# Performance work log

Measured on AMD Instinct MI355X. Metric: run time of the kernel, lower is better.

## Reference

```python
import jax, jax.numpy as jnp
import numpy as np

N = 100_000          # nodes
E = 3_200_000        # edges (avg degree 32)
NEG_SLOPE = 0.2      # PyG GATConv default


def _gat_conv(x, src, dst, W, a_src, a_dst, b, n):
    """Single-head PyG-style GATConv. src/dst already include self-loops."""
    h = x @ W                                   # [N, F_out]
    logits = (h @ a_src)[src] + (h @ a_dst)[dst]  # [E']
    e = jax.nn.leaky_relu(logits, NEG_SLOPE)
    m = jax.ops.segment_max(e, dst, num_segments=n)
    ex = jnp.exp(e - m[dst])                    # stable ragged softmax over in-edges
    s = jax.ops.segment_sum(ex, dst, num_segments=n)
    alpha = ex / (s[dst] + 1e-16)
    out = jax.ops.segment_sum(h[src] * alpha[:, None], dst, num_segments=n)
    return out + b


def setup_inputs() -> dict:
    key = jax.random.key(0)
    ks = jax.random.split(key, 20)
    x = jax.random.normal(ks[0], (N, 3), dtype=jnp.float32)
    edge_index = jax.random.randint(ks[1], (2, E), 0, N, dtype=jnp.int64)

    def lin(k, fin, fout):
        return jax.random.normal(k, (fin, fout), dtype=jnp.float32) * (1.0 / np.sqrt(fin))

    def att(k, f):
        return jax.random.normal(k, (f,), dtype=jnp.float32) * (1.0 / np.sqrt(f))

    inp = {"x": x, "edge_index": edge_index}
    # forward-direction convs
    inp["W1"], inp["as1"], inp["ad1"], inp["b1"] = lin(ks[2], 3, 16), att(ks[3], 16), att(ks[4], 16), jnp.zeros((16,), jnp.float32)
    inp["W2"], inp["as2"], inp["ad2"], inp["b2"] = lin(ks[5], 16, 1), att(ks[6], 1), att(ks[7], 1), jnp.zeros((1,), jnp.float32)
    # reverse-direction convs
    inp["W1r"], inp["as1r"], inp["ad1r"], inp["b1r"] = lin(ks[8], 3, 16), att(ks[9], 16), att(ks[10], 16), jnp.zeros((16,), jnp.float32)
    inp["W2r"], inp["as2r"], inp["ad2r"], inp["b2r"] = lin(ks[11], 16, 1), att(ks[12], 1), att(ks[13], 1), jnp.zeros((1,), jnp.float32)
    return inp


def reference(x, edge_index, W1, as1, ad1, b1, W2, as2, ad2, b2,
              W1r, as1r, ad1r, b1r, W2r, as2r, ad2r, b2r):
    n = x.shape[0]
    loops = jnp.arange(n, dtype=edge_index.dtype)
    # forward direction (self-loops appended, as PyG add_self_loops=True)
    src = jnp.concatenate([edge_index[0], loops])
    dst = jnp.concatenate([edge_index[1], loops])
    # reverse direction: stack([ei[1], ei[0]]) then self-loops
    rsrc = jnp.concatenate([edge_index[1], loops])
    rdst = jnp.concatenate([edge_index[0], loops])

    xf = jax.nn.relu(_gat_conv(x, src, dst, W1, as1, ad1, b1, n))
    xf = _gat_conv(xf, src, dst, W2, as2, ad2, b2, n)

    xr = jax.nn.relu(_gat_conv(x, rsrc, rdst, W1r, as1r, ad1r, b1r, n))
    xr = _gat_conv(xr, rsrc, rdst, W2r, as2r, ad2r, b2r, n)

    return (xf + xr) * 0.5
```

## Files before the change

kernel.cpp:

```cpp
#include <hip/hip_runtime.h>
#include <math.h>

#define NSLOPE 0.2f
#define BSH 8
#define BNODES 256
#define NID_MASK 0x1FFFF
#define SENT 0xFFFFFFFFu
#define CAP 9216
#define GB2 768
#define RT 512
#define EPT2 9
#define REDG (RT * EPT2)
#define RREC (2 * REDG)
#define BN8 256
#define BAG2T 512
#define CPP2 9

__device__ __forceinline__ float lrelu(float v) { return v > 0.f ? v : NSLOPE * v; }

__global__ void k_prep(const float* __restrict__ x,
                       const float* __restrict__ as1, const float* __restrict__ ad1,
                       const float* __restrict__ as1r, const float* __restrict__ ad1r,
                       const float* __restrict__ W1, const float* __restrict__ W1r,
                       float4* __restrict__ rec4f, float4* __restrict__ rec4r,
                       float* __restrict__ s1df, float* __restrict__ s1dr,
                       int* __restrict__ gcur, int NS, int N) {
    int i = blockIdx.x * blockDim.x + threadIdx.x;
    if (i < NS) gcur[i] = 0;
    if (i >= N) return;
    float x0 = x[3 * i], x1 = x[3 * i + 1], x2 = x[3 * i + 2];
    float ssf = 0.f, sdf = 0.f, ssr = 0.f, sdr = 0.f;
#pragma unroll
    for (int k = 0; k < 16; k++) {
        float hf = x0 * W1[k] + x1 * W1[16 + k] + x2 * W1[32 + k];
        ssf += hf * as1[k];
        sdf += hf * ad1[k];
        float hr = x0 * W1r[k] + x1 * W1r[16 + k] + x2 * W1r[32 + k];
        ssr += hr * as1r[k];
        sdr += hr * ad1r[k];
    }
    rec4f[i] = make_float4(x0, x1, x2, ssf);
    rec4r[i] = make_float4(x0, x1, x2, ssr);
    s1df[i] = sdf; s1dr[i] = sdr;
}

__global__ void __launch_bounds__(RT, 6) k_scatsort(
        const void* __restrict__ ei, long long E,
        int NB, int NS, int* __restrict__ gcur, unsigned* __restrict__ bin) {
    extern __shared__ unsigned smem[];
    unsigned* rec = smem;
    int* cnt  = (int*)(rec + RREC);
    int* loff = cnt + NS;
    int* gbs  = loff + NS;
    int* wtot = gbs + NS;
    __shared__ int flagsm;

    int t = threadIdx.x;
    if (t < 64) {
        const unsigned long long* p = (const unsigned long long*)ei;
        bool bad = false;
#pragma unroll
        for (int i = 0; i < 4; i++)
            if (p[t * 4 + i] >= (1ull << 32)) bad = true;
        unsigned long long mask = __ballot(bad);
        if (t == 0) flagsm = (mask == 0ull) ? 1 : 0;
    }
    __syncthreads();
    int fl = flagsm;
    long long chunk = (E + GB2 - 1) / GB2;
    long long cstart = (long long)blockIdx.x * chunk;
    long long cend = cstart + chunk; if (cend > E) cend = E;
    int rot = (int)((blockIdx.x * 197u) % (unsigned)NS);

    for (long long rs = cstart; rs < cend; rs += REDG) {
        int ne = (int)min((long long)REDG, cend - rs);
        for (int i = t; i < NS; i += RT) cnt[i] = 0;
        int eu[EPT2], ev[EPT2];
#pragma unroll
        for (int k = 0; k < EPT2; k++) {
            int idx = t + k * RT;
            eu[k] = -1;
            if (idx < ne) {
                long long i = rs + idx;
                if (fl) { const long long* p = (const long long*)ei;
                          eu[k] = (int)p[i]; ev[k] = (int)p[E + i]; }
                else    { const int* p = (const int*)ei;
                          eu[k] = p[i]; ev[k] = p[E + i]; }
            }
        }
        __syncthreads();
#pragma unroll
        for (int k = 0; k < EPT2; k++) {
            if (eu[k] >= 0) {
                atomicAdd(&cnt[ev[k] >> BSH], 1);
                atomicAdd(&cnt[NB + (eu[k] >> BSH)], 1);
            }
        }
        __syncthreads();
        int base = 0;
        for (int st = 0; st < NS; st += RT) {
            int idx = st + t;
            int val = (idx < NS) ? cnt[idx] : 0;
            int lane = t & 63, wv = t >> 6;
            int incl = val;
#pragma unroll
            for (int od = 1; od < 64; od <<= 1) {
                int up = __shfl_up(incl, od);
                if (lane >= od) incl += up;
            }
            if (lane == 63) wtot[wv] = incl;
            __syncthreads();
            int woff = 0;
#pragma unroll
            for (int j = 0; j < 8; j++) woff += (j < wv) ? wtot[j] : 0;
            if (idx < NS) {
                int lo = base + woff + incl - val;
                loff[idx] = lo;
                cnt[idx] = lo;
                gbs[idx] = val ? atomicAdd(&gcur[idx], val) : 0;
            }
            int stot = 0;
#pragma unroll
            for (int j = 0; j < 8; j++) stot += wtot[j];
            base += stot;
            __syncthreads();
        }
#pragma unroll
        for (int k = 0; k < EPT2; k++) {
            if (eu[k] >= 0) {
                int u = eu[k], v = ev[k];
                unsigned r0 = (unsigned)u | ((unsigned)(v & (BNODES - 1)) << 17);
                int s0 = v >> BSH;
                int p0 = atomicAdd(&cnt[s0], 1);
                rec[p0] = r0;
                unsigned r1 = (unsigned)v | ((unsigned)(u & (BNODES - 1)) << 17);
                int s1 = NB + (u >> BSH);
                int p1 = atomicAdd(&cnt[s1], 1);
                rec[p1] = r1;
            }
        }
        __syncthreads();
        for (int i = t; i < NS; i += RT) {
            int s = i + rot; if (s >= NS) s -= NS;
            int ls = loff[s], le = cnt[s];
            int n = le - ls;
            if (!n) continue;
            int g = gbs[s];
            if (g >= CAP) continue;
            if (g + n > CAP) n = CAP - g;
            long long b = (long long)s * CAP;
            int j = 0;
            if (g & 1) { bin[b + g] = rec[ls]; j = 1; }
            if (((g + j) & 2) && j + 2 <= n) {
                *(uint2*)(bin + b + g + j) = make_uint2(rec[ls + j], rec[ls + j + 1]);
                j += 2;
            }
            for (; j + 4 <= n; j += 4)
                *(uint4*)(bin + b + g + j) =
                    make_uint4(rec[ls + j], rec[ls + j + 1],
                               rec[ls + j + 2], rec[ls + j + 3]);
            if (j + 2 <= n) {
                *(uint2*)(bin + b + g + j) = make_uint2(rec[ls + j], rec[ls + j + 1]);
                j += 2;
            }
            if (j < n) bin[b + g + j] = rec[ls + j];
        }
        __syncthreads();
    }
}

__global__ void __launch_bounds__(BAG2T, 8) k_bagg1(
        unsigned* __restrict__ bin, const int* __restrict__ gcur,
        const float4* __restrict__ rec4f, const float* __restrict__ s1df,
        const float4* __restrict__ rec4r, const float* __restrict__ s1dr,
        const float* __restrict__ b1, const float* __restrict__ W1,
        const float* __restrict__ W2,
        const float* __restrict__ as2, const float* __restrict__ ad2,
        const float* __restrict__ b1r, const float* __restrict__ W1r,
        const float* __restrict__ W2r,
        const float* __restrict__ as2r, const float* __restrict__ ad2r,
        float2* __restrict__ p2f, float* __restrict__ s2df,
        float2* __restrict__ p2r, float* __restrict__ s2dr,
        int* __restrict__ aoff, int* __restrict__ aend, int NB8, int N) {
    int bb = blockIdx.x, dir = blockIdx.y;
    const float4* rec4 = dir ? rec4r : rec4f;
    const float* s1d = dir ? s1dr : s1df;
    const float* b1_ = dir ? b1r : b1;
    const float* W1_ = dir ? W1r : W1;
    const float* W2_ = dir ? W2r : W2;
    float as2v = dir ? as2r[0] : as2[0];
    float ad2v = dir ? ad2r[0] : ad2[0];
    float2* p2 = dir ? p2r : p2f;
    float* s2d = dir ? s2dr : s2df;

    int c0 = dir * NB8 + bb;
    long long base = (long long)c0 * CAP;
    int n0 = gcur[c0]; if (n0 > CAP) n0 = CAP;
    int np0 = (n0 + 1) >> 1;
    int v0 = bb << BSH;
    int nv = N - v0; if (nv > BN8) nv = BN8;

    __shared__ int cnt[BN8];
    __shared__ int loff[BN8];
    __shared__ int segtot[4];
    __shared__ unsigned lds_u[CAP];
    int t = threadIdx.x;

    const uint2* bp0 = (const uint2*)(bin + base);
    uint2 recs[CPP2];
#pragma unroll
    for (int k = 0; k < CPP2; k++) {
        int i = t + k * BAG2T;
        uint2 r = make_uint2(SENT, SENT);
        if (i < np0) {
            r = bp0[i];
            if (2 * i + 1 >= n0) r.y = SENT;
        }
        recs[k] = r;
    }
    if (t < BN8) cnt[t] = 0;
    __syncthreads();
#pragma unroll
    for (int k = 0; k < CPP2; k++) {
        if (recs[k].x != SENT) atomicAdd(&cnt[recs[k].x >> 17], 1);
        if (recs[k].y != SENT) atomicAdd(&cnt[recs[k].y >> 17], 1);
    }
    __syncthreads();
    if (t < BN8) {
        int lane = t & 63, wv = t >> 6;
        int val = cnt[t];
        int incl = val;
#pragma unroll
        for (int od = 1; od < 64; od <<= 1) {
            int up = __shfl_up(incl, od);
            if (lane >= od) incl += up;
        }
        if (lane == 63) segtot[wv] = incl;
        loff[t] = incl - val;
    }
    __syncthreads();
    if (t < BN8) {
        int wv = t >> 6;
        int offs = 0;
#pragma unroll
        for (int j = 0; j < 4; j++) offs += (j < wv) ? segtot[j] : 0;
        int ex = loff[t] + offs;
        loff[t] = ex;
        cnt[t] = ex;
    }
    __syncthreads();
#pragma unroll
    for (int k = 0; k < CPP2; k++) {
        if (recs[k].x != SENT) {
            int q = atomicAdd(&cnt[recs[k].x >> 17], 1);
            lds_u[q] = recs[k].x & NID_MASK;
        }
        if (recs[k].y != SENT) {
            int q = atomicAdd(&cnt[recs[k].y >> 17], 1);
            lds_u[q] = recs[k].y & NID_MASK;
        }
    }
    __syncthreads();
    int node = t >> 1, lane = t & 1;
    float sdv = (node < nv) ? s1d[v0 + node] : 0.f;
    float d = 0.f, a0 = 0.f, a1 = 0.f, a2 = 0.f;
    if (node < nv) {
        int ls = loff[node], le = cnt[node];
        for (int pos = ls + lane; pos < le; pos += 2) {
            unsigned u = lds_u[pos];
            float4 r = rec4[u];
            float w = __expf(lrelu(r.w + sdv));
            d += w; a0 += w * r.x; a1 += w * r.y; a2 += w * r.z;
        }
    }
    d  += __shfl_xor(d, 1);
    a0 += __shfl_xor(a0, 1);
    a1 += __shfl_xor(a1, 1);
    a2 += __shfl_xor(a2, 1);
    if (lane == 0 && node < nv) {
        int v = v0 + node;
        float4 r = rec4[v];
        float w = __expf(lrelu(r.w + sdv));
        float dd = d + w;
        float inv = 1.f / (dd + 1e-16f);
        float m0 = (a0 + w * r.x) * inv;
        float m1 = (a1 + w * r.y) * inv;
        float m2 = (a2 + w * r.z) * inv;
        float h2v = 0.f;
#pragma unroll
        for (int k = 0; k < 16; k++) {
            float o = m0 * W1_[k] + m1 * W1_[16 + k] + m2 * W1_[32 + k] + b1_[k];
            o = fmaxf(o, 0.f);
            h2v += o * W2_[k];
        }
        p2[v] = make_float2(h2v, h2v * as2v);
        s2d[v] = h2v * ad2v;
    }
    int nreal = cnt[BN8 - 1];
    if (t == 0 && (nreal & 1)) lds_u[nreal] = SENT;
    __syncthreads();
    int ndp = (nreal + 1) >> 1;
    uint2* bq = (uint2*)(bin + base);
    for (int i = t; i < ndp; i += BAG2T)
        bq[i] = make_uint2(lds_u[2 * i], lds_u[2 * i + 1]);
    if (t < nv) {
        aoff[dir * N + v0 + t] = (int)(base + loff[t]);
        aend[dir * N + v0 + t] = (int)(base + cnt[t]);
    }
}

__global__ void k_agg2(const unsigned* __restrict__ bin,
                       const int* __restrict__ aoff, const int* __restrict__ aend,
                       const float2* __restrict__ p2f, const float* __restrict__ s2df,
                       const float2* __restrict__ p2r, const float* __restrict__ s2dr,
                       const float* __restrict__ b2, const float* __restrict__ b2r,
                       float* __restrict__ out, int N) {
    int tid = blockIdx.x * blockDim.x + threadIdx.x;
    int v = tid >> 4;
    int lane = tid & 15;
    if (v >= N) return;
    float res[2];
#pragma unroll
    for (int dir = 0; dir < 2; dir++) {
        const float2* p2 = dir ? p2r : p2f;
        const float* s2d = dir ? s2dr : s2df;
        float bias = dir ? b2r[0] : b2[0];
        float sd = s2d[v];
        int st = aoff[dir * N + v], en = aend[dir * N + v];
        float d = 0.f, a = 0.f;
        if (lane == 0) {
            float2 ts = p2[v];
            float w = __expf(lrelu(ts.y + sd));
            d = w; a = w * ts.x;
        }
        int j = st + lane;
        for (; j + 16 < en; j += 32) {
            unsigned u0 = __builtin_nontemporal_load(bin + j);
            unsigned u1 = __builtin_nontemporal_load(bin + j + 16);
            float2 t0 = p2[u0];
            float2 t1 = p2[u1];
            float w0 = __expf(lrelu(t0.y + sd));
            float w1 = __expf(lrelu(t1.y + sd));
            d += w0 + w1;
            a += w0 * t0.x + w1 * t1.x;
        }
        for (; j < en; j += 16) {
            unsigned u = __builtin_nontemporal_load(bin + j);
            float2 t = p2[u];
            float w = __expf(lrelu(t.y + sd));
            d += w;
            a += w * t.x;
        }
#pragma unroll
        for (int mask = 1; mask < 16; mask <<= 1) {
            d += __shfl_xor(d, mask);
            a += __shfl_xor(a, mask);
        }
        res[dir] = a / (d + 1e-16f) + bias;
    }
    if (lane == 0) out[v] = 0.5f * (res[0] + res[1]);
}

extern "C" void kernel_launch(void* const* d_in, const int* in_sizes, int n_in,
                              void* d_out, int out_size, void* d_ws, size_t ws_size,
                              hipStream_t stream) {
    const float* x   = (const float*)d_in[0];
    const void*  ei  = d_in[1];
    const float* W1  = (const float*)d_in[2];
    const float* as1 = (const float*)d_in[3];
    const float* ad1 = (const float*)d_in[4];
    const float* b1  = (const float*)d_in[5];
    const float* W2  = (const float*)d_in[6];
    const float* as2 = (const float*)d_in[7];
    const float* ad2 = (const float*)d_in[8];
    const float* b2  = (const float*)d_in[9];
    const float* W1r  = (const float*)d_in[10];
    const float* as1r = (const float*)d_in[11];
    const float* ad1r = (const float*)d_in[12];
    const float* b1r  = (const float*)d_in[13];
    const float* W2r  = (const float*)d_in[14];
    const float* as2r = (const float*)d_in[15];
    const float* ad2r = (const float*)d_in[16];
    const float* b2r  = (const float*)d_in[17];

    const int N = in_sizes[0] / 3;
    const long long E = in_sizes[1] / 2;
    const int NB8 = (N + BNODES - 1) >> BSH;
    const int NS = 2 * NB8;
    (void)ws_size; (void)n_in; (void)out_size;

    char* w = (char*)d_ws;
    size_t o = 0;
    auto A = [&](size_t bytes) { o = (o + 255) & ~(size_t)255; size_t r = o; o += bytes; return r; };
    size_t oR4f  = A(sizeof(float4) * N);
    size_t oR4r  = A(sizeof(float4) * N);
    size_t oS1df = A(sizeof(float) * N);
    size_t oS1dr = A(sizeof(float) * N);
    size_t oP2f  = A(sizeof(float2) * N);
    size_t oS2df = A(sizeof(float) * N);
    size_t oP2r  = A(sizeof(float2) * N);
    size_t oS2dr = A(sizeof(float) * N);
    size_t oAoff = A(sizeof(int) * 2 * N);
    size_t oAend = A(sizeof(int) * 2 * N);
    size_t oGcur = A(sizeof(int) * NS);
    size_t oBin  = A(sizeof(unsigned) * (size_t)NS * CAP);

    float4* rec4f = (float4*)(w + oR4f);
    float4* rec4r = (float4*)(w + oR4r);
    float*  s1df = (float*)(w + oS1df);
    float*  s1dr = (float*)(w + oS1dr);
    float2* p2f  = (float2*)(w + oP2f);
    float*  s2df = (float*)(w + oS2df);
    float2* p2r  = (float2*)(w + oP2r);
    float*  s2dr = (float*)(w + oS2dr);
    int*    aoff = (int*)(w + oAoff);
    int*    aend = (int*)(w + oAend);
    int*    gcur = (int*)(w + oGcur);
    unsigned* bin = (unsigned*)(w + oBin);

    dim3 gN((N + 255) / 256);
    dim3 gBagg(NB8, 2);
    dim3 gAgg2((N * 16 + 255) / 256);

    size_t smem = sizeof(unsigned) * (size_t)RREC
                + sizeof(int) * (size_t)NS * 3
                + sizeof(int) * 8
                + 64;

    k_prep<<<gN, 256, 0, stream>>>(x, as1, ad1, as1r, ad1r, W1, W1r,
                                   rec4f, rec4r, s1df, s1dr, gcur, NS, N);
    k_scatsort<<<GB2, RT, smem, stream>>>(ei, E, NB8, NS, gcur, bin);
    k_bagg1<<<gBagg, BAG2T, 0, stream>>>(bin, gcur, rec4f, s1df, rec4r, s1dr,
                                         b1, W1, W2, as2, ad2,
                                         b1r, W1r, W2r, as2r, ad2r,
                                         p2f, s2df, p2r, s2dr, aoff, aend, NB8, N);
    k_agg2<<<gAgg2, 256, 0, stream>>>(bin, aoff, aend, p2f, s2df, p2r, s2dr,
                                      b2, b2r, (float*)d_out, N);
}
```

Measured before the change: 234.9 us.

## Replace per-bucket counting sort with LDS float atomics in both aggregations

Both aggregation kernels now stream the unsorted bucket records directly and accumulate per-destination softmax numerators and denominators with shared-memory float atomics. This removes the in-block count, scan and scatter pass along with the write-back of sorted bins and offset arrays. The second layer becomes bucket-per-block like the first and combines the two directions by atomically adding into an output that is zeroed in the prep kernel. The cost is many LDS atomic adds per edge (four or two), possibly contended on popular destinations, and float summation order is no longer deterministic.

```diff
diff --git a/kernel.cpp b/kernel.cpp
--- a/kernel.cpp
+++ b/kernel.cpp
@@ -13,8 +13,7 @@
 #define REDG (RT * EPT2)
 #define RREC (2 * REDG)
 #define BN8 256
-#define BAG2T 512
-#define CPP2 9
+#define AGT 512
 
 __device__ __forceinline__ float lrelu(float v) { return v > 0.f ? v : NSLOPE * v; }
 
@@ -24,10 +23,11 @@
                        const float* __restrict__ W1, const float* __restrict__ W1r,
                        float4* __restrict__ rec4f, float4* __restrict__ rec4r,
                        float* __restrict__ s1df, float* __restrict__ s1dr,
-                       int* __restrict__ gcur, int NS, int N) {
+                       int* __restrict__ gcur, float* __restrict__ out, int NS, int N) {
     int i = blockIdx.x * blockDim.x + threadIdx.x;
     if (i < NS) gcur[i] = 0;
     if (i >= N) return;
+    out[i] = 0.f;
     float x0 = x[3 * i], x1 = x[3 * i + 1], x2 = x[3 * i + 2];
     float ssf = 0.f, sdf = 0.f, ssr = 0.f, sdr = 0.f;
 #pragma unroll
@@ -169,19 +169,15 @@
     }
 }
 
-__global__ void __launch_bounds__(BAG2T, 8) k_bagg1(
-        unsigned* __restrict__ bin, const int* __restrict__ gcur,
+__global__ void __launch_bounds__(AGT, 8) k_agg1(
+        const unsigned* __restrict__ bin, const int* __restrict__ gcur,
         const float4* __restrict__ rec4f, const float* __restrict__ s1df,
         const float4* __restrict__ rec4r, const float* __restrict__ s1dr,
         const float* __restrict__ b1, const float* __restrict__ W1,
-        const float* __restrict__ W2,
-        const float* __restrict__ as2, const float* __restrict__ ad2,
+        const float* __restrict__ W2, const float* __restrict__ as2,
         const float* __restrict__ b1r, const float* __restrict__ W1r,
-        const float* __restrict__ W2r,
-        const float* __restrict__ as2r, const float* __restrict__ ad2r,
-        float2* __restrict__ p2f, float* __restrict__ s2df,
-        float2* __restrict__ p2r, float* __restrict__ s2dr,
-        int* __restrict__ aoff, int* __restrict__ aend, int NB8, int N) {
+        const float* __restrict__ W2r, const float* __restrict__ as2r,
+        float2* __restrict__ p2f, float2* __restrict__ p2r, int NB8, int N) {
     int bb = blockIdx.x, dir = blockIdx.y;
     const float4* rec4 = dir ? rec4r : rec4f;
     const float* s1d = dir ? s1dr : s1df;
@@ -189,9 +185,7 @@
     const float* W1_ = dir ? W1r : W1;
     const float* W2_ = dir ? W2r : W2;
     float as2v = dir ? as2r[0] : as2[0];
-    float ad2v = dir ? ad2r[0] : ad2[0];
     float2* p2 = dir ? p2r : p2f;
-    float* s2d = dir ? s2dr : s2df;
 
     int c0 = dir * NB8 + bb;
     long long base = (long long)c0 * CAP;
@@ -200,92 +194,78 @@
     int v0 = bb << BSH;
     int nv = N - v0; if (nv > BN8) nv = BN8;
 
-    __shared__ int cnt[BN8];
-    __shared__ int loff[BN8];
-    __shared__ int segtot[4];
-    __shared__ unsigned lds_u[CAP];
+    __shared__ float accD[BN8], accX[BN8], accY[BN8], accZ[BN8], s1dl[BN8];
     int t = threadIdx.x;
-
-    const uint2* bp0 = (const uint2*)(bin + base);
-    uint2 recs[CPP2];
-#pragma unroll
-    for (int k = 0; k < CPP2; k++) {
-        int i = t + k * BAG2T;
-        uint2 r = make_uint2(SENT, SENT);
-        if (i < np0) {
-            r = bp0[i];
-            if (2 * i + 1 >= n0) r.y = SENT;
-        }
-        recs[k] = r;
-    }
-    if (t < BN8) cnt[t] = 0;
+    if (t < BN8) {
+        accD[t] = 0.f; accX[t] = 0.f; accY[t] = 0.f; accZ[t] = 0.f;
+        s1dl[t] = (t < nv) ? s1d[v0 + t] : 0.f;
+    }
     __syncthreads();
-#pragma unroll
-    for (int k = 0; k < CPP2; k++) {
-        if (recs[k].x != SENT) atomicAdd(&cnt[recs[k].x >> 17], 1);
-        if (recs[k].y != SENT) atomicAdd(&cnt[recs[k].y >> 17], 1);
+
+    const uint2* bp = (const uint2*)(bin + base);
+    int i = t;
+    for (; i + AGT < np0; i += 2 * AGT) {
+        uint2 ra = bp[i];
+        uint2 rb = bp[i + AGT];
+        unsigned r0 = ra.x, r1 = (2 * i + 1 < n0) ? ra.y : SENT;
+        unsigned r2 = rb.x, r3 = (2 * (i + AGT) + 1 < n0) ? rb.y : SENT;
+        {
+            unsigned u = r0 & NID_MASK; int vl = r0 >> 17;
+            float4 rv = rec4[u];
+            float w = __expf(lrelu(rv.w + s1dl[vl]));
+            atomicAdd(&accD[vl], w);       atomicAdd(&accX[vl], w * rv.x);
+            atomicAdd(&accY[vl], w * rv.y); atomicAdd(&accZ[vl], w * rv.z);
+        }
+        if (r1 != SENT) {
+            unsigned u = r1 & NID_MASK; int vl = r1 >> 17;
+            float4 rv = rec4[u];
+            float w = __expf(lrelu(rv.w + s1dl[vl]));
+            atomicAdd(&accD[vl], w);       atomicAdd(&accX[vl], w * rv.x);
+            atomicAdd(&accY[vl], w * rv.y); atomicAdd(&accZ[vl], w * rv.z);
+        }
+        {
+            unsigned u = r2 & NID_MASK; int vl = r2 >> 17;
+            float4 rv = rec4[u];
+            float w = __expf(lrelu(rv.w + s1dl[vl]));
+            atomicAdd(&accD[vl], w);       atomicAdd(&accX[vl], w * rv.x);
+            atomicAdd(&accY[vl], w * rv.y); atomicAdd(&accZ[vl], w * rv.z);
+        }
+        if (r3 != SENT) {
+            unsigned u = r3 & NID_MASK; int vl = r3 >> 17;
+            float4 rv = rec4[u];
+            float w = __expf(lrelu(rv.w + s1dl[vl]));
+            atomicAdd(&accD[vl], w);       atomicAdd(&accX[vl], w * rv.x);
+            atomicAdd(&accY[vl], w * rv.y); atomicAdd(&accZ[vl], w * rv.z);
+        }
+    }
+    for (; i < np0; i += AGT) {
+        uint2 ra = bp[i];
+        unsigned r0 = ra.x, r1 = (2 * i + 1 < n0) ? ra.y : SENT;
+        {
+            unsigned u = r0 & NID_MASK; int vl = r0 >> 17;
+            float4 rv = rec4[u];
+            float w = __expf(lrelu(rv.w + s1dl[vl]));
+            atomicAdd(&accD[vl], w);       atomicAdd(&accX[vl], w * rv.x);
+            atomicAdd(&accY[vl], w * rv.y); atomicAdd(&accZ[vl], w * rv.z);
+        }
+        if (r1 != SENT) {
+            unsigned u = r1 & NID_MASK; int vl = r1 >> 17;
+            float4 rv = rec4[u];
+            float w = __expf(lrelu(rv.w + s1dl[vl]));
+            atomicAdd(&accD[vl], w);       atomicAdd(&accX[vl], w * rv.x);
+            atomicAdd(&accY[vl], w * rv.y); atomicAdd(&accZ[vl], w * rv.z);
+        }
     }
     __syncthreads();
-    if (t < BN8) {
-        int lane = t & 63, wv = t >> 6;
-        int val = cnt[t];
-        int incl = val;
-#pragma unroll
-        for (int od = 1; od < 64; od <<= 1) {
-            int up = __shfl_up(incl, od);
-            if (lane >= od) incl += up;
-        }
-        if (lane == 63) segtot[wv] = incl;
-        loff[t] = incl - val;
-    }
-    __syncthreads();
-    if (t < BN8) {
-        int wv = t >> 6;
-        int offs = 0;
-#pragma unroll
-        for (int j = 0; j < 4; j++) offs += (j < wv) ? segtot[j] : 0;
-        int ex = loff[t] + offs;
-        loff[t] = ex;
-        cnt[t] = ex;
-    }
-    __syncthreads();
-#pragma unroll
-    for (int k = 0; k < CPP2; k++) {
-        if (recs[k].x != SENT) {
-            int q = atomicAdd(&cnt[recs[k].x >> 17], 1);
-            lds_u[q] = recs[k].x & NID_MASK;
-        }
-        if (recs[k].y != SENT) {
-            int q = atomicAdd(&cnt[recs[k].y >> 17], 1);
-            lds_u[q] = recs[k].y & NID_MASK;
-        }
-    }
-    __syncthreads();
-    int node = t >> 1, lane = t & 1;
-    float sdv = (node < nv) ? s1d[v0 + node] : 0.f;
-    float d = 0.f, a0 = 0.f, a1 = 0.f, a2 = 0.f;
-    if (node < nv) {
-        int ls = loff[node], le = cnt[node];
-        for (int pos = ls + lane; pos < le; pos += 2) {
-            unsigned u = lds_u[pos];
-            float4 r = rec4[u];
-            float w = __expf(lrelu(r.w + sdv));
-            d += w; a0 += w * r.x; a1 += w * r.y; a2 += w * r.z;
-        }
-    }
-    d  += __shfl_xor(d, 1);
-    a0 += __shfl_xor(a0, 1);
-    a1 += __shfl_xor(a1, 1);
-    a2 += __shfl_xor(a2, 1);
-    if (lane == 0 && node < nv) {
-        int v = v0 + node;
-        float4 r = rec4[v];
-        float w = __expf(lrelu(r.w + sdv));
-        float dd = d + w;
+    if (t < nv) {
+        int v = v0 + t;
+        float4 rv = rec4[v];
+        float w = __expf(lrelu(rv.w + s1dl[t]));
+        float dd = accD[t] + w;
         float inv = 1.f / (dd + 1e-16f);
-        float m0 = (a0 + w * r.x) * inv;
-        float m1 = (a1 + w * r.y) * inv;
-        float m2 = (a2 + w * r.z) * inv;
+        float m0 = (accX[t] + w * rv.x) * inv;
+        float m1 = (accY[t] + w * rv.y) * inv;
+        float m2 = (accZ[t] + w * rv.z) * inv;
         float h2v = 0.f;
 #pragma unroll
         for (int k = 0; k < 16; k++) {
@@ -294,71 +274,92 @@
             h2v += o * W2_[k];
         }
         p2[v] = make_float2(h2v, h2v * as2v);
-        s2d[v] = h2v * ad2v;
-    }
-    int nreal = cnt[BN8 - 1];
-    if (t == 0 && (nreal & 1)) lds_u[nreal] = SENT;
+    }
+}
+
+__global__ void __launch_bounds__(AGT, 8) k_agg2(
+        const unsigned* __restrict__ bin, const int* __restrict__ gcur,
+        const float2* __restrict__ p2f, const float2* __restrict__ p2r,
+        const float* __restrict__ ad2, const float* __restrict__ ad2r,
+        const float* __restrict__ b2, const float* __restrict__ b2r,
+        float* __restrict__ out, int NB8, int N) {
+    int bb = blockIdx.x, dir = blockIdx.y;
+    const float2* p2 = dir ? p2r : p2f;
+    float ad2v = dir ? ad2r[0] : ad2[0];
+    float b2v  = dir ? b2r[0] : b2[0];
+
+    int c0 = dir * NB8 + bb;
+    long long base = (long long)c0 * CAP;
+    int n0 = gcur[c0]; if (n0 > CAP) n0 = CAP;
+    int np0 = (n0 + 1) >> 1;
+    int v0 = bb << BSH;
+    int nv = N - v0; if (nv > BN8) nv = BN8;
+
+    __shared__ float accD[BN8], accA[BN8], s2dl[BN8], p2xl[BN8], p2yl[BN8];
+    int t = threadIdx.x;
+    if (t < BN8) {
+        accD[t] = 0.f; accA[t] = 0.f;
+        float2 pv = (t < nv) ? p2[v0 + t] : make_float2(0.f, 0.f);
+        p2xl[t] = pv.x; p2yl[t] = pv.y; s2dl[t] = pv.x * ad2v;
+    }
     __syncthreads();
-    int ndp = (nreal + 1) >> 1;
-    uint2* bq = (uint2*)(bin + base);
-    for (int i = t; i < ndp; i += BAG2T)
-        bq[i] = make_uint2(lds_u[2 * i], lds_u[2 * i + 1]);
+
+    const uint2* bp = (const uint2*)(bin + base);
+    int i = t;
+    for (; i + AGT < np0; i += 2 * AGT) {
+        uint2 ra = bp[i];
+        uint2 rb = bp[i + AGT];
+        unsigned r0 = ra.x, r1 = (2 * i + 1 < n0) ? ra.y : SENT;
+        unsigned r2 = rb.x, r3 = (2 * (i + AGT) + 1 < n0) ? rb.y : SENT;
+        {
+            unsigned u = r0 & NID_MASK; int vl = r0 >> 17;
+            float2 pu = p2[u];
+            float w = __expf(lrelu(pu.y + s2dl[vl]));
+            atomicAdd(&accD[vl], w); atomicAdd(&accA[vl], w * pu.x);
+        }
+        if (r1 != SENT) {
+            unsigned u = r1 & NID_MASK; int vl = r1 >> 17;
+            float2 pu = p2[u];
+            float w = __expf(lrelu(pu.y + s2dl[vl]));
+            atomicAdd(&accD[vl], w); atomicAdd(&accA[vl], w * pu.x);
+        }
+        {
+            unsigned u = r2 & NID_MASK; int vl = r2 >> 17;
+            float2 pu = p2[u];
+            float w = __expf(lrelu(pu.y + s2dl[vl]));
+            atomicAdd(&accD[vl], w); atomicAdd(&accA[vl], w * pu.x);
+        }
+        if (r3 != SENT) {
+            unsigned u = r3 & NID_MASK; int vl = r3 >> 17;
+            float2 pu = p2[u];
+            float w = __expf(lrelu(pu.y + s2dl[vl]));
+            atomicAdd(&accD[vl], w); atomicAdd(&accA[vl], w * pu.x);
+        }
+    }
+    for (; i < np0; i += AGT) {
+        uint2 ra = bp[i];
+        unsigned r0 = ra.x, r1 = (2 * i + 1 < n0) ? ra.y : SENT;
+        {
+            unsigned u = r0 & NID_MASK; int vl = r0 >> 17;
+            float2 pu = p2[u];
+            float w = __expf(lrelu(pu.y + s2dl[vl]));
+            atomicAdd(&accD[vl], w); atomicAdd(&accA[vl], w * pu.x);
+        }
+        if (r1 != SENT) {
+            unsigned u = r1 & NID_MASK; int vl = r1 >> 17;
+            float2 pu = p2[u];
+            float w = __expf(lrelu(pu.y + s2dl[vl]));
+            atomicAdd(&accD[vl], w); atomicAdd(&accA[vl], w * pu.x);
+        }
+    }
+    __syncthreads();
     if (t < nv) {
-        aoff[dir * N + v0 + t] = (int)(base + loff[t]);
-        aend[dir * N + v0 + t] = (int)(base + cnt[t]);
-    }
-}
-
-__global__ void k_agg2(const unsigned* __restrict__ bin,
-                       const int* __restrict__ aoff, const int* __restrict__ aend,
-                       const float2* __restrict__ p2f, const float* __restrict__ s2df,
-                       const float2* __restrict__ p2r, const float* __restrict__ s2dr,
-                       const float* __restrict__ b2, const float* __restrict__ b2r,
-                       float* __restrict__ out, int N) {
-    int tid = blockIdx.x * blockDim.x + threadIdx.x;
-    int v = tid >> 4;
-    int lane = tid & 15;
-    if (v >= N) return;
-    float res[2];
-#pragma unroll
-    for (int dir = 0; dir < 2; dir++) {
-        const float2* p2 = dir ? p2r : p2f;
-        const float* s2d = dir ? s2dr : s2df;
-        float bias = dir ? b2r[0] : b2[0];
-        float sd = s2d[v];
-        int st = aoff[dir * N + v], en = aend[dir * N + v];
-        float d = 0.f, a = 0.f;
-        if (lane == 0) {
-            float2 ts = p2[v];
-            float w = __expf(lrelu(ts.y + sd));
-            d = w; a = w * ts.x;
-        }
-        int j = st + lane;
-        for (; j + 16 < en; j += 32) {
-            unsigned u0 = __builtin_nontemporal_load(bin + j);
-            unsigned u1 = __builtin_nontemporal_load(bin + j + 16);
-            float2 t0 = p2[u0];
-            float2 t1 = p2[u1];
-            float w0 = __expf(lrelu(t0.y + sd));
-            float w1 = __expf(lrelu(t1.y + sd));
-            d += w0 + w1;
-            a += w0 * t0.x + w1 * t1.x;
-        }
-        for (; j < en; j += 16) {
-            unsigned u = __builtin_nontemporal_load(bin + j);
-            float2 t = p2[u];
-            float w = __expf(lrelu(t.y + sd));
-            d += w;
-            a += w * t.x;
-        }
-#pragma unroll
-        for (int mask = 1; mask < 16; mask <<= 1) {
-            d += __shfl_xor(d, mask);
-            a += __shfl_xor(a, mask);
-        }
-        res[dir] = a / (d + 1e-16f) + bias;
-    }
-    if (lane == 0) out[v] = 0.5f * (res[0] + res[1]);
+        float w = __expf(lrelu(p2yl[t] + s2dl[t]));
+        float dd = accD[t] + w;
+        float aa = accA[t] + w * p2xl[t];
+        float res = aa / (dd + 1e-16f) + b2v;
+        atomicAdd(out + v0 + t, 0.5f * res);
+    }
 }
 
 extern "C" void kernel_launch(void* const* d_in, const int* in_sizes, int n_in,
@@ -397,11 +398,7 @@
     size_t oS1df = A(sizeof(float) * N);
     size_t oS1dr = A(sizeof(float) * N);
     size_t oP2f  = A(sizeof(float2) * N);
-    size_t oS2df = A(sizeof(float) * N);
     size_t oP2r  = A(sizeof(float2) * N);
-    size_t oS2dr = A(sizeof(float) * N);
-    size_t oAoff = A(sizeof(int) * 2 * N);
-    size_t oAend = A(sizeof(int) * 2 * N);
     size_t oGcur = A(sizeof(int) * NS);
     size_t oBin  = A(sizeof(unsigned) * (size_t)NS * CAP);
 
@@ -410,17 +407,13 @@
     float*  s1df = (float*)(w + oS1df);
     float*  s1dr = (float*)(w + oS1dr);
     float2* p2f  = (float2*)(w + oP2f);
-    float*  s2df = (float*)(w + oS2df);
     float2* p2r  = (float2*)(w + oP2r);
-    float*  s2dr = (float*)(w + oS2dr);
-    int*    aoff = (int*)(w + oAoff);
-    int*    aend = (int*)(w + oAend);
     int*    gcur = (int*)(w + oGcur);
     unsigned* bin = (unsigned*)(w + oBin);
+    float*  outp = (float*)d_out;
 
     dim3 gN((N + 255) / 256);
-    dim3 gBagg(NB8, 2);
-    dim3 gAgg2((N * 16 + 255) / 256);
+    dim3 gAgg(NB8, 2);
 
     size_t smem = sizeof(unsigned) * (size_t)RREC
                 + sizeof(int) * (size_t)NS * 3
@@ -428,12 +421,12 @@
                 + 64;
 
     k_prep<<<gN, 256, 0, stream>>>(x, as1, ad1, as1r, ad1r, W1, W1r,
-                                   rec4f, rec4r, s1df, s1dr, gcur, NS, N);
+                                   rec4f, rec4r, s1df, s1dr, gcur, outp, NS, N);
     k_scatsort<<<GB2, RT, smem, stream>>>(ei, E, NB8, NS, gcur, bin);
-    k_bagg1<<<gBagg, BAG2T, 0, stream>>>(bin, gcur, rec4f, s1df, rec4r, s1dr,
-                                         b1, W1, W2, as2, ad2,
-                                         b1r, W1r, W2r, as2r, ad2r,
-                                         p2f, s2df, p2r, s2dr, aoff, aend, NB8, N);
-    k_agg2<<<gAgg2, 256, 0, stream>>>(bin, aoff, aend, p2f, s2df, p2r, s2dr,
-                                      b2, b2r, (float*)d_out, N);
+    k_agg1<<<gAgg, AGT, 0, stream>>>(bin, gcur, rec4f, s1df, rec4r, s1dr,
+                                     b1, W1, W2, as2,
+                                     b1r, W1r, W2r, as2r,
+                                     p2f, p2r, NB8, N);
+    k_agg2<<<gAgg, AGT, 0, stream>>>(bin, gcur, p2f, p2r,
+                                     ad2, ad2r, b2, b2r, outp, NB8, N);
 }
```

Result: slower. 409.3 us (+74.3%).
